# Kernel optimization log

Measured on AMD Instinct MI355X. Metric: run time of the kernel, lower is better.

Reference implementation:

```python
import jax, jax.numpy as jnp
import numpy as np

N_SEQ, N_RES, C_M = 1024, 768, 64
NUM_HEAD = 8
HEAD_DIM = C_M // NUM_HEAD  # key_dim == value_dim == 8 per head
LARGE = 1e9
LN_EPS = 1e-5
MEAN_EPS = 1e-10


def setup_inputs() -> dict:
    key = jax.random.key(0)
    ks = jax.random.split(key, 8)
    msa_act = jax.random.normal(ks[0], (N_SEQ, N_RES, C_M), dtype=jnp.float32)
    msa_mask = (jax.random.uniform(ks[1], (N_SEQ, N_RES)) > 0.15).astype(jnp.float32)
    # fan-avg uniform init like VarianceScaling(1.0, 'fan_avg', 'uniform')
    def vs(k, shape, fan_in, fan_out):
        limit = jnp.sqrt(3.0 * 2.0 / (fan_in + fan_out))
        return jax.random.uniform(k, shape, minval=-limit, maxval=limit, dtype=jnp.float32)
    return {
        "msa_act": msa_act,
        "msa_mask": msa_mask,
        "ln_scale": jnp.ones((C_M,), jnp.float32),
        "ln_bias": jnp.zeros((C_M,), jnp.float32),
        "query_w": vs(ks[2], (C_M, NUM_HEAD, HEAD_DIM), C_M, NUM_HEAD * HEAD_DIM),
        "key_w": vs(ks[3], (C_M, HEAD_DIM), C_M, HEAD_DIM),
        "value_w": vs(ks[4], (C_M, HEAD_DIM), C_M, HEAD_DIM),
        "gating_w": jnp.zeros((C_M, NUM_HEAD, HEAD_DIM), jnp.float32),
        "gating_b": jnp.ones((NUM_HEAD, HEAD_DIM), jnp.float32),
        "output_w": vs(ks[5], (NUM_HEAD, HEAD_DIM, C_M), NUM_HEAD * HEAD_DIM, C_M),
        "output_b": jnp.zeros((C_M,), jnp.float32),
    }


def reference(msa_act, msa_mask, ln_scale, ln_bias, query_w, key_w, value_w,
              gating_w, gating_b, output_w, output_b):
    # permute: columns become the batch axis b = N_res
    x = jnp.transpose(msa_act, (1, 0, 2))          # [R, S, C]
    mask = jnp.transpose(msa_mask, (1, 0))[..., None]  # [R, S, 1]

    # LayerNorm over channels
    mu = jnp.mean(x, axis=-1, keepdims=True)
    var = jnp.mean(jnp.square(x - mu), axis=-1, keepdims=True)
    x = (x - mu) * jax.lax.rsqrt(var + LN_EPS) * ln_scale + ln_bias

    # shared (non-per-head) K/V projections
    v = jnp.einsum('bka,ac->bkc', x, value_w)      # [R, S, d]
    k = jnp.einsum('bka,ac->bkc', x, key_w)        # [R, S, d]

    # masked-mean single query per column
    q_avg = jnp.sum(mask * x, axis=1) / (jnp.sum(mask, axis=1) + MEAN_EPS)  # [R, C]
    q = jnp.einsum('ba,ahc->bhc', q_avg, query_w) * (HEAD_DIM ** -0.5)      # [R, H, d]

    bias = LARGE * (mask[:, None, :, 0] - 1.0)     # [R, 1, S]
    logits = jnp.einsum('bhc,bkc->bhk', q, k) + bias
    weights = jax.nn.softmax(logits, axis=-1)      # [R, H, S]
    weighted_avg = jnp.einsum('bhk,bkc->bhc', weights, v)  # [R, H, d]

    # sigmoid gating per (query, head, channel)
    gate = jax.nn.sigmoid(jnp.einsum('bqc,chv->bqhv', x, gating_w) + gating_b)  # [R, S, H, d]
    gated = weighted_avg[:, None] * gate           # [R, S, H, d]
    out = jnp.einsum('bqhc,hco->bqo', gated, output_w) + output_b  # [R, S, C]

    return jnp.transpose(out, (1, 0, 2))           # [S, R, C]
```

## Files before the change

### kernel.cpp

```cpp
#include <hip/hip_runtime.h>
#include <hip/hip_bf16.h>

#define N_S 1024
#define N_R 768
#define LN_EPS 1e-5f
#define MEAN_EPS 1e-10f
#define LARGE_F 1e9f
#define QSCALE 0.35355339059327373f

typedef __attribute__((ext_vector_type(8))) __bf16 bf16x8;
typedef __attribute__((ext_vector_type(4))) float f32x4;

__device__ __forceinline__ float bflo(unsigned u){ union{unsigned v; float f;} x; x.v = u << 16; return x.f; }
__device__ __forceinline__ unsigned short f2b(float f){
  __hip_bfloat16 h = __float2bfloat16(f);
  return *reinterpret_cast<unsigned short*>(&h);
}
__device__ __forceinline__ unsigned pk2(float a, float b){
  return (unsigned)f2b(a) | ((unsigned)f2b(b) << 16);
}
__device__ __forceinline__ bf16x8 ld_frag(const void* p){
  uint4 u = *reinterpret_cast<const uint4*>(p);
  return __builtin_bit_cast(bf16x8, u);
}

struct SharedS { _Float16 kv[N_S][16]; };

__global__ __launch_bounds__(256, 2) void stats_kernel(
    const float* __restrict__ act, const float* __restrict__ mask,
    const float* __restrict__ lns, const float* __restrict__ lnb,
    const float* __restrict__ qw,  const float* __restrict__ kw,
    const float* __restrict__ vw,  const float* __restrict__ gw,
    const float* __restrict__ ow,  float* __restrict__ wavg_out,
    uint4* __restrict__ wsf)
{
  __shared__ SharedS sh;
  __shared__ float redA[4][64];
  __shared__ float redB[4][8];
  __shared__ float q_lds[64];
  __shared__ float qf_lds[64];

  const int tid  = threadIdx.x;
  const int lane = tid & 63;
  const int wave = tid >> 6;
  const int r    = blockIdx.x;

  if (r >= N_R) {
    #pragma unroll 1
    for (int rep = 0; rep < 2; rep++) {
      int fi = wave + rep * 4;
      int mf = fi >> 1, ks = fi & 1;
      int g = lane >> 4, c15 = lane & 15;
      union { uint4 u; unsigned short h[8]; } ghi, glo, ohi, olo;
      #pragma unroll
      for (int t = 0; t < 8; t++) {
        int k = ks * 32 + g * 8 + t;
        float gv = gw[k * 64 + mf * 16 + c15];
        unsigned short gh = f2b(gv);
        ghi.h[t] = gh;
        glo.h[t] = f2b(gv - bflo(gh));
        float ov = ow[k * 64 + mf * 16 + c15];
        unsigned short oh = f2b(ov);
        ohi.h[t] = oh;
        olo.h[t] = f2b(ov - bflo(oh));
      }
      wsf[(0 * 8 + fi) * 64 + lane] = ghi.u;
      wsf[(1 * 8 + fi) * 64 + lane] = glo.u;
      wsf[(2 * 8 + fi) * 64 + lane] = ohi.u;
      wsf[(3 * 8 + fi) * 64 + lane] = olo.u;
    }
    return;
  }

  float qacc[64];
  #pragma unroll
  for (int c = 0; c < 64; c++) qacc[c] = 0.f;
  float msum = 0.f;

  #pragma unroll 1
  for (int it = 0; it < 4; it++) {
    int s = tid + it * 256;
    size_t base = ((size_t)s * N_R + r) * 64;
    float rw[64];
    const float4* rp = reinterpret_cast<const float4*>(act + base);
    #pragma unroll
    for (int i = 0; i < 16; i++) reinterpret_cast<float4*>(rw)[i] = rp[i];

    float m = mask[(size_t)s * N_R + r];

    float sum = 0.f, ss = 0.f;
    #pragma unroll
    for (int c = 0; c < 64; c++) { sum += rw[c]; ss += rw[c] * rw[c]; }
    float mu  = sum * (1.f / 64.f);
    float var = ss * (1.f / 64.f) - mu * mu;
    float rsd = rsqrtf(var + LN_EPS);

    float kacc[8], vacc[8];
    #pragma unroll
    for (int d = 0; d < 8; d++) { kacc[d] = 0.f; vacc[d] = 0.f; }

    #pragma unroll
    for (int c = 0; c < 64; c++) {
      float xn = fmaf((rw[c] - mu) * rsd, lns[c], lnb[c]);
      qacc[c] = fmaf(m, xn, qacc[c]);
      #pragma unroll
      for (int d = 0; d < 8; d++) {
        kacc[d] = fmaf(xn, kw[c * 8 + d], kacc[d]);
        vacc[d] = fmaf(xn, vw[c * 8 + d], vacc[d]);
      }
    }
    union { uint4 u; _Float16 h[8]; } kb, vb;
    #pragma unroll
    for (int d = 0; d < 8; d++) { kb.h[d] = (_Float16)kacc[d]; vb.h[d] = (_Float16)vacc[d]; }
    *reinterpret_cast<uint4*>(&sh.kv[s][0]) = kb.u;
    *reinterpret_cast<uint4*>(&sh.kv[s][8]) = vb.u;
    msum += m;
  }

  #pragma unroll
  for (int c = 0; c < 64; c++) {
    #pragma unroll
    for (int o = 32; o > 0; o >>= 1) qacc[c] += __shfl_xor(qacc[c], o);
  }
  #pragma unroll
  for (int o = 32; o > 0; o >>= 1) msum += __shfl_xor(msum, o);
  if (lane == 0) {
    redB[wave][0] = msum;
    #pragma unroll
    for (int c = 0; c < 64; c++) redA[wave][c] = qacc[c];
  }
  __syncthreads();
  if (tid < 64) {
    float qs = redA[0][tid] + redA[1][tid] + redA[2][tid] + redA[3][tid];
    float mt = redB[0][0] + redB[1][0] + redB[2][0] + redB[3][0];
    q_lds[tid] = qs / (mt + MEAN_EPS);
  }
  __syncthreads();
  if (tid < 64) {
    float acc = 0.f;
    for (int c = 0; c < 64; c++) acc = fmaf(q_lds[c], qw[c * 64 + tid], acc);
    qf_lds[tid] = acc * QSCALE;
  }
  __syncthreads();

  float qreg[64];
  #pragma unroll
  for (int j = 0; j < 64; j++) qreg[j] = qf_lds[j];

  float ev[4][8];
  float hm[8];
  #pragma unroll
  for (int h = 0; h < 8; h++) hm[h] = -1e30f;

  #pragma unroll
  for (int it = 0; it < 4; it++) {
    int s = tid + it * 256;
    union { uint4 u; _Float16 h[8]; } kb;
    kb.u = *reinterpret_cast<uint4*>(&sh.kv[s][0]);
    float kk[8];
    #pragma unroll
    for (int d = 0; d < 8; d++) kk[d] = (float)kb.h[d];
    float m = mask[(size_t)s * N_R + r];
    float bias = LARGE_F * (m - 1.f);
    #pragma unroll
    for (int h = 0; h < 8; h++) {
      float l = bias;
      #pragma unroll
      for (int d = 0; d < 8; d++) l = fmaf(qreg[h * 8 + d], kk[d], l);
      ev[it][h] = l;
      hm[h] = fmaxf(hm[h], l);
    }
  }
  #pragma unroll
  for (int h = 0; h < 8; h++) {
    #pragma unroll
    for (int o = 32; o > 0; o >>= 1) hm[h] = fmaxf(hm[h], __shfl_xor(hm[h], o));
  }
  if (lane == 0) {
    #pragma unroll
    for (int h = 0; h < 8; h++) redB[wave][h] = hm[h];
  }
  __syncthreads();
  #pragma unroll
  for (int h = 0; h < 8; h++)
    hm[h] = fmaxf(fmaxf(redB[0][h], redB[1][h]), fmaxf(redB[2][h], redB[3][h]));
  __syncthreads();

  float hs[8];
  #pragma unroll
  for (int h = 0; h < 8; h++) hs[h] = 0.f;
  #pragma unroll
  for (int it = 0; it < 4; it++) {
    #pragma unroll
    for (int h = 0; h < 8; h++) {
      float e = __expf(ev[it][h] - hm[h]);
      ev[it][h] = e;
      hs[h] += e;
    }
  }
  #pragma unroll
  for (int h = 0; h < 8; h++) {
    #pragma unroll
    for (int o = 32; o > 0; o >>= 1) hs[h] += __shfl_xor(hs[h], o);
  }
  if (lane == 0) {
    #pragma unroll
    for (int h = 0; h < 8; h++) redB[wave][h] = hs[h];
  }
  __syncthreads();

  float wacc[64];
  #pragma unroll
  for (int j = 0; j < 64; j++) wacc[j] = 0.f;
  #pragma unroll
  for (int it = 0; it < 4; it++) {
    int s = tid + it * 256;
    union { uint4 u; _Float16 h[8]; } vb;
    vb.u = *reinterpret_cast<uint4*>(&sh.kv[s][8]);
    float vv[8];
    #pragma unroll
    for (int d = 0; d < 8; d++) vv[d] = (float)vb.h[d];
    #pragma unroll
    for (int h = 0; h < 8; h++) {
      float w = ev[it][h];
      #pragma unroll
      for (int d = 0; d < 8; d++) wacc[h * 8 + d] = fmaf(w, vv[d], wacc[h * 8 + d]);
    }
  }
  #pragma unroll
  for (int j = 0; j < 64; j++) {
    #pragma unroll
    for (int o = 32; o > 0; o >>= 1) wacc[j] += __shfl_xor(wacc[j], o);
  }
  if (lane == 0) {
    #pragma unroll
    for (int j = 0; j < 64; j++) redA[wave][j] = wacc[j];
  }
  __syncthreads();
  if (tid < 64) {
    int h = tid >> 3;
    float hsv = redB[0][h] + redB[1][h] + redB[2][h] + redB[3][h];
    wavg_out[r * 64 + tid] =
        (redA[0][tid] + redA[1][tid] + redA[2][tid] + redA[3][tid]) / hsv;
  }
}

__global__ __launch_bounds__(256, 2) void proj_kernel(
    const float* __restrict__ act, const float* __restrict__ lns,
    const float* __restrict__ lnb, const float* __restrict__ gb,
    const float* __restrict__ ob,  const float* __restrict__ wavg,
    const uint4* __restrict__ wsf, float* __restrict__ out)
{
  __shared__ uint4 wfrag[32][64];
  __shared__ __align__(16) char wbuf[4][4096];

  const int tid  = threadIdx.x;
  const int lane = tid & 63;
  const int wv   = tid >> 6;
  const int r    = blockIdx.x >> 4;
  const int s0   = ((blockIdx.x & 15) << 6) + wv * 16;

  {
    uint4* dst = &wfrag[0][0];
    #pragma unroll
    for (int i = 0; i < 8; i++) dst[tid + i * 256] = wsf[tid + i * 256];
  }
  __syncthreads();

  char* my = wbuf[wv];
  const int qr = lane >> 2, qc = lane & 3;

  const size_t rowbase = ((size_t)(s0 + qr) * N_R + r) * 64;

  float rv[16];
  {
    const float4* ap = reinterpret_cast<const float4*>(act + rowbase);
    #pragma unroll
    for (int i = 0; i < 4; i++)
      *reinterpret_cast<float4*>(&rv[4 * i]) = ap[qc + 4 * i];
  }
  float sum = 0.f, ssq = 0.f;
  #pragma unroll
  for (int j = 0; j < 16; j++) { sum += rv[j]; ssq += rv[j] * rv[j]; }
  sum += __shfl_xor(sum, 1); ssq += __shfl_xor(ssq, 1);
  sum += __shfl_xor(sum, 2); ssq += __shfl_xor(ssq, 2);
  float mu  = sum * (1.f / 64.f);
  float rsd = rsqrtf(ssq * (1.f / 64.f) - mu * mu + LN_EPS);

  #pragma unroll
  for (int i = 0; i < 4; i++) {
    int c0 = 16 * i + 4 * qc;
    float4 s4 = *reinterpret_cast<const float4*>(lns + c0);
    float4 b4 = *reinterpret_cast<const float4*>(lnb + c0);
    float x0 = fmaf((rv[4*i+0] - mu) * rsd, s4.x, b4.x);
    float x1 = fmaf((rv[4*i+1] - mu) * rsd, s4.y, b4.y);
    float x2 = fmaf((rv[4*i+2] - mu) * rsd, s4.z, b4.z);
    float x3 = fmaf((rv[4*i+3] - mu) * rsd, s4.w, b4.w);
    uint2 p; p.x = pk2(x0, x1); p.y = pk2(x2, x3);
    int byt = ((2 * i + (qc >> 1)) << 8) + (qr << 4) + ((qc & 1) << 3);
    *reinterpret_cast<uint2*>(my + byt) = p;
  }
  asm volatile("" ::: "memory");
  bf16x8 xb0 = ld_frag(my + lane * 16);
  bf16x8 xb1 = ld_frag(my + 1024 + lane * 16);

  const f32x4 zero = {0.f, 0.f, 0.f, 0.f};
  f32x4 acc[4] = {zero, zero, zero, zero};
  #pragma unroll
  for (int mf = 0; mf < 4; mf++) {
    acc[mf] = __builtin_amdgcn_mfma_f32_16x16x32_bf16(ld_frag(&wfrag[     mf*2    ][lane]), xb0, acc[mf], 0, 0, 0);
    acc[mf] = __builtin_amdgcn_mfma_f32_16x16x32_bf16(ld_frag(&wfrag[ 8 + mf*2    ][lane]), xb0, acc[mf], 0, 0, 0);
    acc[mf] = __builtin_amdgcn_mfma_f32_16x16x32_bf16(ld_frag(&wfrag[     mf*2 + 1][lane]), xb1, acc[mf], 0, 0, 0);
    acc[mf] = __builtin_amdgcn_mfma_f32_16x16x32_bf16(ld_frag(&wfrag[ 8 + mf*2 + 1][lane]), xb1, acc[mf], 0, 0, 0);
  }

  const int g = lane >> 4, c15 = lane & 15;
  asm volatile("" ::: "memory");
  #pragma unroll
  for (int mf = 0; mf < 4; mf++) {
    int jb = mf * 16 + 4 * g;
    float4 wv4 = *reinterpret_cast<const float4*>(wavg + r * 64 + jb);
    float4 gb4 = *reinterpret_cast<const float4*>(gb + jb);
    float c0 = wv4.x / (1.f + __expf(-(acc[mf][0] + gb4.x)));
    float c1 = wv4.y / (1.f + __expf(-(acc[mf][1] + gb4.y)));
    float c2 = wv4.z / (1.f + __expf(-(acc[mf][2] + gb4.z)));
    float c3 = wv4.w / (1.f + __expf(-(acc[mf][3] + gb4.w)));
    uint2 p; p.x = pk2(c0, c1); p.y = pk2(c2, c3);
    int byt = 2048 + ((2 * mf + (g >> 1)) << 8) + (c15 << 4) + ((g & 1) << 3);
    *reinterpret_cast<uint2*>(my + byt) = p;
  }
  asm volatile("" ::: "memory");
  bf16x8 cb0 = ld_frag(my + 2048 + lane * 16);
  bf16x8 cb1 = ld_frag(my + 3072 + lane * 16);

  f32x4 acc2[4] = {zero, zero, zero, zero};
  #pragma unroll
  for (int mf = 0; mf < 4; mf++) {
    acc2[mf] = __builtin_amdgcn_mfma_f32_16x16x32_bf16(ld_frag(&wfrag[16 + mf*2    ][lane]), cb0, acc2[mf], 0, 0, 0);
    acc2[mf] = __builtin_amdgcn_mfma_f32_16x16x32_bf16(ld_frag(&wfrag[24 + mf*2    ][lane]), cb0, acc2[mf], 0, 0, 0);
    acc2[mf] = __builtin_amdgcn_mfma_f32_16x16x32_bf16(ld_frag(&wfrag[16 + mf*2 + 1][lane]), cb1, acc2[mf], 0, 0, 0);
    acc2[mf] = __builtin_amdgcn_mfma_f32_16x16x32_bf16(ld_frag(&wfrag[24 + mf*2 + 1][lane]), cb1, acc2[mf], 0, 0, 0);
  }

  asm volatile("" ::: "memory");
  #pragma unroll
  for (int mf = 0; mf < 4; mf++) {
    int o0 = mf * 16 + 4 * g;
    float4 ob4 = *reinterpret_cast<const float4*>(ob + o0);
    float4 o4;
    o4.x = acc2[mf][0] + ob4.x;
    o4.y = acc2[mf][1] + ob4.y;
    o4.z = acc2[mf][2] + ob4.z;
    o4.w = acc2[mf][3] + ob4.w;
    *reinterpret_cast<float4*>(my + (c15 << 8) + (o0 << 2)) = o4;
  }
  asm volatile("" ::: "memory");
  {
    float4* op = reinterpret_cast<float4*>(out + rowbase);
    #pragma unroll
    for (int i = 0; i < 4; i++)
      op[qc + 4 * i] = *reinterpret_cast<const float4*>(my + (qr << 8) + ((qc + 4 * i) << 4));
  }
}

extern "C" void kernel_launch(void* const* d_in, const int* in_sizes, int n_in,
                              void* d_out, int out_size, void* d_ws, size_t ws_size,
                              hipStream_t stream)
{
  const float* act  = (const float*)d_in[0];
  const float* mask = (const float*)d_in[1];
  const float* lns  = (const float*)d_in[2];
  const float* lnb  = (const float*)d_in[3];
  const float* qw   = (const float*)d_in[4];
  const float* kw   = (const float*)d_in[5];
  const float* vw   = (const float*)d_in[6];
  const float* gw   = (const float*)d_in[7];
  const float* gb   = (const float*)d_in[8];
  const float* ow   = (const float*)d_in[9];
  const float* ob   = (const float*)d_in[10];

  float* wavg_ws = (float*)d_ws;
  uint4* wsf     = (uint4*)((char*)d_ws + N_R * 64 * sizeof(float));

  stats_kernel<<<N_R + 1, 256, 0, stream>>>(act, mask, lns, lnb, qw, kw, vw,
                                            gw, ow, wavg_ws, wsf);
  proj_kernel<<<N_R * 16, 256, 0, stream>>>(act, lns, lnb, gb, ob,
                                            wavg_ws, (const uint4*)wsf, (float*)d_out);
}
```

Measured before the change: 545.2 us.

## Split stats into parallel LN/KV and softmax kernels; persistent double-buffered projection

```diff
diff --git a/kernel.cpp b/kernel.cpp
--- a/kernel.cpp
+++ b/kernel.cpp
@@ -22,6 +22,259 @@
 __device__ __forceinline__ bf16x8 ld_frag(const void* p){
   uint4 u = *reinterpret_cast<const uint4*>(p);
   return __builtin_bit_cast(bf16x8, u);
+}
+
+__device__ __forceinline__ void weight_prep(int wave, int lane,
+    const float* __restrict__ gw, const float* __restrict__ ow, uint4* __restrict__ wsf)
+{
+  #pragma unroll 1
+  for (int rep = 0; rep < 2; rep++) {
+    int fi = wave + rep * 4;
+    int mf = fi >> 1, ks = fi & 1;
+    int g = lane >> 4, c15 = lane & 15;
+    union { uint4 u; unsigned short h[8]; } ghi, glo, ohi, olo;
+    #pragma unroll
+    for (int t = 0; t < 8; t++) {
+      int k = ks * 32 + g * 8 + t;
+      float gv = gw[k * 64 + mf * 16 + c15];
+      unsigned short gh = f2b(gv);
+      ghi.h[t] = gh;
+      glo.h[t] = f2b(gv - bflo(gh));
+      float ov = ow[k * 64 + mf * 16 + c15];
+      unsigned short oh = f2b(ov);
+      ohi.h[t] = oh;
+      olo.h[t] = f2b(ov - bflo(oh));
+    }
+    wsf[(0 * 8 + fi) * 64 + lane] = ghi.u;
+    wsf[(1 * 8 + fi) * 64 + lane] = glo.u;
+    wsf[(2 * 8 + fi) * 64 + lane] = ohi.u;
+    wsf[(3 * 8 + fi) * 64 + lane] = olo.u;
+  }
+}
+
+__global__ __launch_bounds__(256, 4) void lnkv_kernel(
+    const float* __restrict__ act, const float* __restrict__ mask,
+    const float* __restrict__ lns, const float* __restrict__ lnb,
+    const float* __restrict__ kw,  const float* __restrict__ vw,
+    const float* __restrict__ gw,  const float* __restrict__ ow,
+    _Float16* __restrict__ kvws,   float* __restrict__ qpart,
+    float* __restrict__ mpart,     uint4* __restrict__ wsf)
+{
+  __shared__ float redA[4][64];
+  __shared__ float redB[4];
+
+  const int tid  = threadIdx.x;
+  const int lane = tid & 63;
+  const int wave = tid >> 6;
+  const int b    = blockIdx.x;
+
+  if (b >= 3072) { weight_prep(wave, lane, gw, ow, wsf); return; }
+
+  const int r  = b >> 2;
+  const int sc = b & 3;
+  const int s  = sc * 256 + tid;
+
+  size_t base = ((size_t)s * N_R + r) * 64;
+  float rw[64];
+  const float4* rp = reinterpret_cast<const float4*>(act + base);
+  #pragma unroll
+  for (int i = 0; i < 16; i++) reinterpret_cast<float4*>(rw)[i] = rp[i];
+  float m = mask[(size_t)s * N_R + r];
+
+  float sum = 0.f, ss = 0.f;
+  #pragma unroll
+  for (int c = 0; c < 64; c++) { sum += rw[c]; ss += rw[c] * rw[c]; }
+  float mu  = sum * (1.f / 64.f);
+  float rsd = rsqrtf(ss * (1.f / 64.f) - mu * mu + LN_EPS);
+
+  float kacc[8], vacc[8];
+  #pragma unroll
+  for (int d = 0; d < 8; d++) { kacc[d] = 0.f; vacc[d] = 0.f; }
+  #pragma unroll
+  for (int c = 0; c < 64; c++) {
+    float xn = fmaf((rw[c] - mu) * rsd, lns[c], lnb[c]);
+    rw[c] = xn;
+    #pragma unroll
+    for (int d = 0; d < 8; d++) {
+      kacc[d] = fmaf(xn, kw[c * 8 + d], kacc[d]);
+      vacc[d] = fmaf(xn, vw[c * 8 + d], vacc[d]);
+    }
+  }
+  {
+    union { uint4 u; _Float16 h[8]; } kb, vb;
+    #pragma unroll
+    for (int d = 0; d < 8; d++) { kb.h[d] = (_Float16)kacc[d]; vb.h[d] = (_Float16)vacc[d]; }
+    _Float16* kvp = kvws + ((size_t)r * N_S + s) * 16;
+    *reinterpret_cast<uint4*>(kvp)     = kb.u;
+    *reinterpret_cast<uint4*>(kvp + 8) = vb.u;
+  }
+
+  float v[32];
+  {
+    const bool hi = (lane & 32) != 0;
+    #pragma unroll
+    for (int i = 0; i < 32; i++) {
+      float gave = m * (hi ? rw[i] : rw[i + 32]);
+      float keep = m * (hi ? rw[i + 32] : rw[i]);
+      v[i] = keep + __shfl_xor(gave, 32);
+    }
+  }
+  #pragma unroll
+  for (int half = 16; half >= 1; half >>= 1) {
+    const bool hi = (lane & half) != 0;
+    #pragma unroll
+    for (int i = 0; i < half; i++) {
+      float gave = hi ? v[i] : v[i + half];
+      float keep = hi ? v[i + half] : v[i];
+      v[i] = keep + __shfl_xor(gave, half);
+    }
+  }
+  float ms = m;
+  #pragma unroll
+  for (int o = 32; o > 0; o >>= 1) ms += __shfl_xor(ms, o);
+
+  redA[wave][lane] = v[0];
+  if (lane == 0) redB[wave] = ms;
+  __syncthreads();
+  if (tid < 64)
+    qpart[((size_t)sc * N_R + r) * 64 + tid] =
+        redA[0][tid] + redA[1][tid] + redA[2][tid] + redA[3][tid];
+  if (tid == 64)
+    mpart[sc * N_R + r] = redB[0] + redB[1] + redB[2] + redB[3];
+}
+
+__global__ __launch_bounds__(256, 2) void softmax_kernel(
+    const float* __restrict__ mask, const float* __restrict__ qpart,
+    const float* __restrict__ mpart, const float* __restrict__ qw,
+    const _Float16* __restrict__ kvws, float* __restrict__ wavg_out)
+{
+  __shared__ float redA[4][64];
+  __shared__ float redB[4][8];
+  __shared__ float q_lds[64];
+  __shared__ float qf_lds[64];
+
+  const int tid  = threadIdx.x;
+  const int lane = tid & 63;
+  const int wave = tid >> 6;
+  const int r    = blockIdx.x;
+
+  if (tid < 64) {
+    float qs = qpart[((size_t)0 * N_R + r) * 64 + tid] +
+               qpart[((size_t)1 * N_R + r) * 64 + tid] +
+               qpart[((size_t)2 * N_R + r) * 64 + tid] +
+               qpart[((size_t)3 * N_R + r) * 64 + tid];
+    float mt = mpart[0 * N_R + r] + mpart[1 * N_R + r] +
+               mpart[2 * N_R + r] + mpart[3 * N_R + r];
+    q_lds[tid] = qs / (mt + MEAN_EPS);
+  }
+  __syncthreads();
+  if (tid < 64) {
+    float acc = 0.f;
+    for (int c = 0; c < 64; c++) acc = fmaf(q_lds[c], qw[c * 64 + tid], acc);
+    qf_lds[tid] = acc * QSCALE;
+  }
+  __syncthreads();
+
+  float qreg[64];
+  #pragma unroll
+  for (int j = 0; j < 64; j++) qreg[j] = qf_lds[j];
+
+  float ev[4][8];
+  float hm[8];
+  #pragma unroll
+  for (int h = 0; h < 8; h++) hm[h] = -1e30f;
+
+  #pragma unroll
+  for (int it = 0; it < 4; it++) {
+    int s = tid + it * 256;
+    union { uint4 u; _Float16 h[8]; } kb;
+    kb.u = *reinterpret_cast<const uint4*>(kvws + ((size_t)r * N_S + s) * 16);
+    float kk[8];
+    #pragma unroll
+    for (int d = 0; d < 8; d++) kk[d] = (float)kb.h[d];
+    float m = mask[(size_t)s * N_R + r];
+    float bias = LARGE_F * (m - 1.f);
+    #pragma unroll
+    for (int h = 0; h < 8; h++) {
+      float l = bias;
+      #pragma unroll
+      for (int d = 0; d < 8; d++) l = fmaf(qreg[h * 8 + d], kk[d], l);
+      ev[it][h] = l;
+      hm[h] = fmaxf(hm[h], l);
+    }
+  }
+  #pragma unroll
+  for (int h = 0; h < 8; h++) {
+    #pragma unroll
+    for (int o = 32; o > 0; o >>= 1) hm[h] = fmaxf(hm[h], __shfl_xor(hm[h], o));
+  }
+  if (lane == 0) {
+    #pragma unroll
+    for (int h = 0; h < 8; h++) redB[wave][h] = hm[h];
+  }
+  __syncthreads();
+  #pragma unroll
+  for (int h = 0; h < 8; h++)
+    hm[h] = fmaxf(fmaxf(redB[0][h], redB[1][h]), fmaxf(redB[2][h], redB[3][h]));
+  __syncthreads();
+
+  float hs[8];
+  #pragma unroll
+  for (int h = 0; h < 8; h++) hs[h] = 0.f;
+  #pragma unroll
+  for (int it = 0; it < 4; it++) {
+    #pragma unroll
+    for (int h = 0; h < 8; h++) {
+      float e = __expf(ev[it][h] - hm[h]);
+      ev[it][h] = e;
+      hs[h] += e;
+    }
+  }
+  #pragma unroll
+  for (int h = 0; h < 8; h++) {
+    #pragma unroll
+    for (int o = 32; o > 0; o >>= 1) hs[h] += __shfl_xor(hs[h], o);
+  }
+  if (lane == 0) {
+    #pragma unroll
+    for (int h = 0; h < 8; h++) redB[wave][h] = hs[h];
+  }
+  __syncthreads();
+
+  float wacc[64];
+  #pragma unroll
+  for (int j = 0; j < 64; j++) wacc[j] = 0.f;
+  #pragma unroll
+  for (int it = 0; it < 4; it++) {
+    int s = tid + it * 256;
+    union { uint4 u; _Float16 h[8]; } vb;
+    vb.u = *reinterpret_cast<const uint4*>(kvws + ((size_t)r * N_S + s) * 16 + 8);
+    float vv[8];
+    #pragma unroll
+    for (int d = 0; d < 8; d++) vv[d] = (float)vb.h[d];
+    #pragma unroll
+    for (int h = 0; h < 8; h++) {
+      float w = ev[it][h];
+      #pragma unroll
+      for (int d = 0; d < 8; d++) wacc[h * 8 + d] = fmaf(w, vv[d], wacc[h * 8 + d]);
+    }
+  }
+  #pragma unroll
+  for (int j = 0; j < 64; j++) {
+    #pragma unroll
+    for (int o = 32; o > 0; o >>= 1) wacc[j] += __shfl_xor(wacc[j], o);
+  }
+  if (lane == 0) {
+    #pragma unroll
+    for (int j = 0; j < 64; j++) redA[wave][j] = wacc[j];
+  }
+  __syncthreads();
+  if (tid < 64) {
+    int h = tid >> 3;
+    float hsv = redB[0][h] + redB[1][h] + redB[2][h] + redB[3][h];
+    wavg_out[r * 64 + tid] =
+        (redA[0][tid] + redA[1][tid] + redA[2][tid] + redA[3][tid]) / hsv;
+  }
 }
 
 struct SharedS { _Float16 kv[N_S][16]; };
@@ -45,32 +298,7 @@
   const int wave = tid >> 6;
   const int r    = blockIdx.x;
 
-  if (r >= N_R) {
-    #pragma unroll 1
-    for (int rep = 0; rep < 2; rep++) {
-      int fi = wave + rep * 4;
-      int mf = fi >> 1, ks = fi & 1;
-      int g = lane >> 4, c15 = lane & 15;
-      union { uint4 u; unsigned short h[8]; } ghi, glo, ohi, olo;
-      #pragma unroll
-      for (int t = 0; t < 8; t++) {
-        int k = ks * 32 + g * 8 + t;
-        float gv = gw[k * 64 + mf * 16 + c15];
-        unsigned short gh = f2b(gv);
-        ghi.h[t] = gh;
-        glo.h[t] = f2b(gv - bflo(gh));
-        float ov = ow[k * 64 + mf * 16 + c15];
-        unsigned short oh = f2b(ov);
-        ohi.h[t] = oh;
-        olo.h[t] = f2b(ov - bflo(oh));
-      }
-      wsf[(0 * 8 + fi) * 64 + lane] = ghi.u;
-      wsf[(1 * 8 + fi) * 64 + lane] = glo.u;
-      wsf[(2 * 8 + fi) * 64 + lane] = ohi.u;
-      wsf[(3 * 8 + fi) * 64 + lane] = olo.u;
-    }
-    return;
-  }
+  if (r >= N_R) { weight_prep(wave, lane, gw, ow, wsf); return; }
 
   float qacc[64];
   #pragma unroll
@@ -85,20 +313,15 @@
     const float4* rp = reinterpret_cast<const float4*>(act + base);
     #pragma unroll
     for (int i = 0; i < 16; i++) reinterpret_cast<float4*>(rw)[i] = rp[i];
-
     float m = mask[(size_t)s * N_R + r];
-
     float sum = 0.f, ss = 0.f;
     #pragma unroll
     for (int c = 0; c < 64; c++) { sum += rw[c]; ss += rw[c] * rw[c]; }
     float mu  = sum * (1.f / 64.f);
-    float var = ss * (1.f / 64.f) - mu * mu;
-    float rsd = rsqrtf(var + LN_EPS);
-
+    float rsd = rsqrtf(ss * (1.f / 64.f) - mu * mu + LN_EPS);
     float kacc[8], vacc[8];
     #pragma unroll
     for (int d = 0; d < 8; d++) { kacc[d] = 0.f; vacc[d] = 0.f; }
-
     #pragma unroll
     for (int c = 0; c < 64; c++) {
       float xn = fmaf((rw[c] - mu) * rsd, lns[c], lnb[c]);
@@ -146,12 +369,10 @@
   float qreg[64];
   #pragma unroll
   for (int j = 0; j < 64; j++) qreg[j] = qf_lds[j];
-
   float ev[4][8];
   float hm[8];
   #pragma unroll
   for (int h = 0; h < 8; h++) hm[h] = -1e30f;
-
   #pragma unroll
   for (int it = 0; it < 4; it++) {
     int s = tid + it * 256;
@@ -245,43 +466,22 @@
   }
 }
 
-__global__ __launch_bounds__(256, 2) void proj_kernel(
-    const float* __restrict__ act, const float* __restrict__ lns,
-    const float* __restrict__ lnb, const float* __restrict__ gb,
-    const float* __restrict__ ob,  const float* __restrict__ wavg,
-    const uint4* __restrict__ wsf, float* __restrict__ out)
+__device__ __forceinline__ void proj_tile(
+    const float4 (&rv)[4], int t, int wv, int lane, int qr, int qc, int g, int c15,
+    const float4 (&s4)[4], const float4 (&b4)[4],
+    const float* __restrict__ gb, const float* __restrict__ ob,
+    const float* __restrict__ wavg, const uint4 (*wfrag)[64],
+    char* my, float* __restrict__ out)
 {
-  __shared__ uint4 wfrag[32][64];
-  __shared__ __align__(16) char wbuf[4][4096];
-
-  const int tid  = threadIdx.x;
-  const int lane = tid & 63;
-  const int wv   = tid >> 6;
-  const int r    = blockIdx.x >> 4;
-  const int s0   = ((blockIdx.x & 15) << 6) + wv * 16;
-
-  {
-    uint4* dst = &wfrag[0][0];
-    #pragma unroll
-    for (int i = 0; i < 8; i++) dst[tid + i * 256] = wsf[tid + i * 256];
-  }
-  __syncthreads();
-
-  char* my = wbuf[wv];
-  const int qr = lane >> 2, qc = lane & 3;
-
-  const size_t rowbase = ((size_t)(s0 + qr) * N_R + r) * 64;
-
-  float rv[16];
-  {
-    const float4* ap = reinterpret_cast<const float4*>(act + rowbase);
-    #pragma unroll
-    for (int i = 0; i < 4; i++)
-      *reinterpret_cast<float4*>(&rv[4 * i]) = ap[qc + 4 * i];
-  }
+  const int r  = t >> 4;
+  const int s0 = ((t & 15) << 6) + wv * 16;
+
   float sum = 0.f, ssq = 0.f;
   #pragma unroll
-  for (int j = 0; j < 16; j++) { sum += rv[j]; ssq += rv[j] * rv[j]; }
+  for (int i = 0; i < 4; i++) {
+    sum += rv[i].x + rv[i].y + rv[i].z + rv[i].w;
+    ssq += rv[i].x * rv[i].x + rv[i].y * rv[i].y + rv[i].z * rv[i].z + rv[i].w * rv[i].w;
+  }
   sum += __shfl_xor(sum, 1); ssq += __shfl_xor(ssq, 1);
   sum += __shfl_xor(sum, 2); ssq += __shfl_xor(ssq, 2);
   float mu  = sum * (1.f / 64.f);
@@ -289,13 +489,10 @@
 
   #pragma unroll
   for (int i = 0; i < 4; i++) {
-    int c0 = 16 * i + 4 * qc;
-    float4 s4 = *reinterpret_cast<const float4*>(lns + c0);
-    float4 b4 = *reinterpret_cast<const float4*>(lnb + c0);
-    float x0 = fmaf((rv[4*i+0] - mu) * rsd, s4.x, b4.x);
-    float x1 = fmaf((rv[4*i+1] - mu) * rsd, s4.y, b4.y);
-    float x2 = fmaf((rv[4*i+2] - mu) * rsd, s4.z, b4.z);
-    float x3 = fmaf((rv[4*i+3] - mu) * rsd, s4.w, b4.w);
+    float x0 = fmaf((rv[i].x - mu) * rsd, s4[i].x, b4[i].x);
+    float x1 = fmaf((rv[i].y - mu) * rsd, s4[i].y, b4[i].y);
+    float x2 = fmaf((rv[i].z - mu) * rsd, s4[i].z, b4[i].z);
+    float x3 = fmaf((rv[i].w - mu) * rsd, s4[i].w, b4[i].w);
     uint2 p; p.x = pk2(x0, x1); p.y = pk2(x2, x3);
     int byt = ((2 * i + (qc >> 1)) << 8) + (qr << 4) + ((qc & 1) << 3);
     *reinterpret_cast<uint2*>(my + byt) = p;
@@ -314,7 +511,6 @@
     acc[mf] = __builtin_amdgcn_mfma_f32_16x16x32_bf16(ld_frag(&wfrag[ 8 + mf*2 + 1][lane]), xb1, acc[mf], 0, 0, 0);
   }
 
-  const int g = lane >> 4, c15 = lane & 15;
   asm volatile("" ::: "memory");
   #pragma unroll
   for (int mf = 0; mf < 4; mf++) {
@@ -326,12 +522,12 @@
     float c2 = wv4.z / (1.f + __expf(-(acc[mf][2] + gb4.z)));
     float c3 = wv4.w / (1.f + __expf(-(acc[mf][3] + gb4.w)));
     uint2 p; p.x = pk2(c0, c1); p.y = pk2(c2, c3);
-    int byt = 2048 + ((2 * mf + (g >> 1)) << 8) + (c15 << 4) + ((g & 1) << 3);
+    int byt = ((2 * mf + (g >> 1)) << 8) + (c15 << 4) + ((g & 1) << 3);
     *reinterpret_cast<uint2*>(my + byt) = p;
   }
   asm volatile("" ::: "memory");
-  bf16x8 cb0 = ld_frag(my + 2048 + lane * 16);
-  bf16x8 cb1 = ld_frag(my + 3072 + lane * 16);
+  bf16x8 cb0 = ld_frag(my + lane * 16);
+  bf16x8 cb1 = ld_frag(my + 1024 + lane * 16);
 
   f32x4 acc2[4] = {zero, zero, zero, zero};
   #pragma unroll
@@ -342,24 +538,76 @@
     acc2[mf] = __builtin_amdgcn_mfma_f32_16x16x32_bf16(ld_frag(&wfrag[24 + mf*2 + 1][lane]), cb1, acc2[mf], 0, 0, 0);
   }
 
-  asm volatile("" ::: "memory");
+  size_t obase = ((size_t)(s0 + c15) * N_R + r) * 64;
   #pragma unroll
   for (int mf = 0; mf < 4; mf++) {
     int o0 = mf * 16 + 4 * g;
-    float4 ob4 = *reinterpret_cast<const float4*>(ob + o0);
+    float4 e = *reinterpret_cast<const float4*>(ob + o0);
     float4 o4;
-    o4.x = acc2[mf][0] + ob4.x;
-    o4.y = acc2[mf][1] + ob4.y;
-    o4.z = acc2[mf][2] + ob4.z;
-    o4.w = acc2[mf][3] + ob4.w;
-    *reinterpret_cast<float4*>(my + (c15 << 8) + (o0 << 2)) = o4;
-  }
-  asm volatile("" ::: "memory");
+    o4.x = acc2[mf][0] + e.x;
+    o4.y = acc2[mf][1] + e.y;
+    o4.z = acc2[mf][2] + e.z;
+    o4.w = acc2[mf][3] + e.w;
+    *reinterpret_cast<float4*>(out + obase + o0) = o4;
+  }
+}
+
+__global__ __launch_bounds__(256, 4) void proj_kernel(
+    const float* __restrict__ act, const float* __restrict__ lns,
+    const float* __restrict__ lnb, const float* __restrict__ gb,
+    const float* __restrict__ ob,  const float* __restrict__ wavg,
+    const uint4* __restrict__ wsf, float* __restrict__ out)
+{
+  __shared__ uint4 wfrag[32][64];
+  __shared__ __align__(16) char wbuf[4][2048];
+
+  const int tid  = threadIdx.x;
+  const int lane = tid & 63;
+  const int wv   = tid >> 6;
+  const int b    = blockIdx.x;
+  const int qr = lane >> 2, qc = lane & 3;
+  const int g = lane >> 4, c15 = lane & 15;
+  char* my = wbuf[wv];
+
+  float4 rvA[4], rvB[4];
   {
-    float4* op = reinterpret_cast<float4*>(out + rowbase);
-    #pragma unroll
-    for (int i = 0; i < 4; i++)
-      op[qc + 4 * i] = *reinterpret_cast<const float4*>(my + (qr << 8) + ((qc + 4 * i) << 4));
+    int t = b;
+    const float4* ap = reinterpret_cast<const float4*>(
+        act + ((size_t)((((t & 15) << 6) + wv * 16) + qr) * N_R + (t >> 4)) * 64);
+    rvA[0] = ap[qc]; rvA[1] = ap[qc + 4]; rvA[2] = ap[qc + 8]; rvA[3] = ap[qc + 12];
+  }
+
+  {
+    uint4* dst = &wfrag[0][0];
+    #pragma unroll
+    for (int i = 0; i < 8; i++) dst[tid + i * 256] = wsf[tid + i * 256];
+  }
+
+  float4 s4[4], b4[4];
+  #pragma unroll
+  for (int i = 0; i < 4; i++) {
+    int c0 = 16 * i + 4 * qc;
+    s4[i] = *reinterpret_cast<const float4*>(lns + c0);
+    b4[i] = *reinterpret_cast<const float4*>(lnb + c0);
+  }
+  __syncthreads();
+
+  #pragma unroll 1
+  for (int i = 0; i < 12; i += 2) {
+    {
+      int t = (i + 1) * 1024 + b;
+      const float4* ap = reinterpret_cast<const float4*>(
+          act + ((size_t)((((t & 15) << 6) + wv * 16) + qr) * N_R + (t >> 4)) * 64);
+      rvB[0] = ap[qc]; rvB[1] = ap[qc + 4]; rvB[2] = ap[qc + 8]; rvB[3] = ap[qc + 12];
+    }
+    proj_tile(rvA, i * 1024 + b, wv, lane, qr, qc, g, c15, s4, b4, gb, ob, wavg, wfrag, my, out);
+    if (i + 2 < 12) {
+      int t = (i + 2) * 1024 + b;
+      const float4* ap = reinterpret_cast<const float4*>(
+          act + ((size_t)((((t & 15) << 6) + wv * 16) + qr) * N_R + (t >> 4)) * 64);
+      rvA[0] = ap[qc]; rvA[1] = ap[qc + 4]; rvA[2] = ap[qc + 8]; rvA[3] = ap[qc + 12];
+    }
+    proj_tile(rvB, (i + 1) * 1024 + b, wv, lane, qr, qc, g, c15, s4, b4, gb, ob, wavg, wfrag, my, out);
   }
 }
 
@@ -376,14 +624,28 @@
   const float* vw   = (const float*)d_in[6];
   const float* gw   = (const float*)d_in[7];
   const float* gb   = (const float*)d_in[8];
+  const float* ob   = (const float*)d_in[10];
   const float* ow   = (const float*)d_in[9];
-  const float* ob   = (const float*)d_in[10];
-
-  float* wavg_ws = (float*)d_ws;
-  uint4* wsf     = (uint4*)((char*)d_ws + N_R * 64 * sizeof(float));
-
-  stats_kernel<<<N_R + 1, 256, 0, stream>>>(act, mask, lns, lnb, qw, kw, vw,
-                                            gw, ow, wavg_ws, wsf);
-  proj_kernel<<<N_R * 16, 256, 0, stream>>>(act, lns, lnb, gb, ob,
-                                            wavg_ws, (const uint4*)wsf, (float*)d_out);
-}
+
+  char* ws = (char*)d_ws;
+  float* wavg_ws = (float*)ws;
+  uint4* wsf     = (uint4*)(ws + 196608);
+  const size_t OFF_KV = 229376;
+  const size_t OFF_QP = OFF_KV + 25165824;
+  const size_t OFF_MP = OFF_QP + 786432;
+  const size_t NEED   = OFF_MP + 12288;
+
+  if (ws_size >= NEED) {
+    _Float16* kvws = (_Float16*)(ws + OFF_KV);
+    float* qpart   = (float*)(ws + OFF_QP);
+    float* mpart   = (float*)(ws + OFF_MP);
+    lnkv_kernel<<<3073, 256, 0, stream>>>(act, mask, lns, lnb, kw, vw, gw, ow,
+                                          kvws, qpart, mpart, wsf);
+    softmax_kernel<<<N_R, 256, 0, stream>>>(mask, qpart, mpart, qw, kvws, wavg_ws);
+  } else {
+    stats_kernel<<<N_R + 1, 256, 0, stream>>>(act, mask, lns, lnb, qw, kw, vw,
+                                              gw, ow, wavg_ws, wsf);
+  }
+  proj_kernel<<<1024, 256, 0, stream>>>(act, lns, lnb, gb, ob,
+                                        wavg_ws, (const uint4*)wsf, (float*)d_out);
+}
```

New measurement: 649.9 us. +19.2%, slower.
